# Optimization experiments

Measured on AMD Instinct MI355X. Metric: run time of the kernel, lower is better.

Reference implementation:

```python
import jax, jax.numpy as jnp
import numpy as np

# Model hyper-parameters (from CMRET __init__ defaults)
N_A, F, H, K, NK, L = 4096, 128, 4, 15, 50, 6
CUTOFF, TEMP, BOX, N_Z = 5.0, 2.0, 40.0, 100
DH = F // H  # per-head dim


def setup_inputs() -> dict:
    key = jax.random.key(0)
    ks = jax.random.split(key, 12)
    Z = jax.random.randint(ks[0], (1, N_A), 0, N_Z)
    R = jax.random.uniform(ks[1], (1, N_A, 3), dtype=jnp.float32) * BOX
    batch = jnp.ones((1, N_A, 1), jnp.float32)
    g = lambda k, shp, s: jax.random.normal(k, shp, jnp.float32) * s
    emb = g(ks[2], (N_Z, F), 1.0)
    Wq = g(ks[3], (L, F, F), F ** -0.5)
    Wk = g(ks[4], (L, F, F), F ** -0.5)
    Wv = g(ks[5], (L, F, 3 * F), F ** -0.5)
    We_k = g(ks[6], (L, NK, F), NK ** -0.5)
    be_k = jnp.zeros((L, F), jnp.float32)
    We_v = g(ks[7], (L, NK, 3 * F), NK ** -0.5)
    be_v = jnp.zeros((L, 3 * F), jnp.float32)
    ln_g = jnp.ones((F,), jnp.float32)
    ln_b = jnp.zeros((F,), jnp.float32)
    Wo1 = g(ks[8], (F, F), F ** -0.5)
    Wo2 = g(ks[9], (F, 1), F ** -0.5)
    return dict(Z=Z, R=R, batch=batch, emb=emb, Wq=Wq, Wk=Wk, Wv=Wv,
                We_k=We_k, be_k=be_k, We_v=We_v, be_v=be_v,
                ln_g=ln_g, ln_b=ln_b, Wo1=Wo1, Wo2=Wo2)


def reference(Z, R, batch, emb, Wq, Wk, Wv, We_k, be_k, We_v, be_v, ln_g, ln_b, Wo1, Wo2):
    n_a = Z.shape[1]
    r = R[0]                                  # (n_a, 3)
    b = batch[..., 0]                         # (1, n_a)
    bm = (b.T @ b) == 0                       # (n_a, n_a) cross-molecule mask
    # --- Distance: k-nearest-neighbour selection (gather-based) ---
    sq = jnp.sum(r * r, -1)
    d2 = sq[:, None] + sq[None, :] - 2.0 * (r @ r.T)
    d2 = jnp.where(bm | jnp.eye(n_a, dtype=bool), 1e9, jnp.maximum(d2, 0.0))
    _, idxs = jax.lax.top_k(-d2, K)           # (n_a, K) neighbour indices
    vec = r[idxs] - r[:, None, :]             # (n_a, K, 3)
    d = jnp.sqrt(jnp.sum(vec * vec, -1) + 1e-12)
    vec_norm = vec / d[..., None]
    # --- Gaussian RBF * cosine cutoff edge features ---
    mu = jnp.linspace(0.0, CUTOFF, NK, dtype=jnp.float32)
    delta = CUTOFF / NK
    cut = 0.5 * (jnp.cos(jnp.pi * d / CUTOFF) + 1.0) * (d <= CUTOFF)
    e = jnp.exp(-((d[..., None] - mu) ** 2) / (2.0 * delta * delta)) * cut[..., None]
    # --- embedding and channel init ---
    s = emb[Z[0]]                             # (n_a, F) scalar channel
    o = jnp.zeros_like(s)                     # residual accumulator
    v = jnp.zeros((n_a, 3, F), s.dtype)       # vector channel
    scale = jnp.asarray(1.0 / np.sqrt(DH * TEMP), jnp.float32)
    # --- attention interaction stack ---
    for l in range(L):
        q = (s @ Wq[l]).reshape(n_a, H, DH)
        kk = s @ Wk[l]
        val = s @ Wv[l]                       # (n_a, 3F)
        ek = jax.nn.silu(e @ We_k[l] + be_k[l])   # (n_a, K, F) edge key filter
        ev = jax.nn.silu(e @ We_v[l] + be_v[l])   # (n_a, K, 3F) edge value filter
        kh = (kk[idxs] * ek).reshape(n_a, K, H, DH)
        logits = jnp.einsum('nhd,nkhd->nkh', q, kh) * scale
        attn = jax.nn.softmax(logits, axis=1) * cut[..., None]
        wf = jnp.repeat(attn, DH, axis=-1)        # (n_a, K, F) per-channel weights
        m1, m2, m3 = jnp.split(val[idxs] * ev, 3, axis=-1)
        ds = jnp.sum(wf * m1, axis=1)             # scalar message (n_a, F)
        dv = jnp.sum((wf * m2)[:, :, None, :] * vec_norm[..., None]
                     + (wf * m3)[:, :, None, :] * v[idxs], axis=1)
        s = s + ds
        o = o + ds
        v = v + dv
    # --- final LayerNorm + readout ---
    mean = o.mean(-1, keepdims=True)
    var = o.var(-1, keepdims=True)
    o = (o - mean) / jnp.sqrt(var + 1e-5) * ln_g + ln_b
    h = jax.nn.silu(o @ Wo1) @ Wo2            # (n_a, 1) per-atom contribution
    return jnp.sum(h * batch[0], axis=0, keepdims=True)  # (1, 1) energy
```

## Files before the change

### kernel.cpp

```cpp
#include <hip/hip_runtime.h>
#include <math.h>

#define NATOMS  4096
#define FDIM    128
#define NHEAD   4
#define DHEAD   32
#define KNBR    15
#define NKER    50
#define NLAYER  6
#define QKVW    640
#define LISTCAP 768

typedef __attribute__((ext_vector_type(8))) short short8;
typedef __attribute__((ext_vector_type(4))) float f32x4;

__device__ __forceinline__ float silu_f(float x) { return x / (1.0f + __expf(-x)); }

__device__ __forceinline__ unsigned long long shfl_xor_u64(unsigned long long v, int m) {
    unsigned lo = (unsigned)v, hi = (unsigned)(v >> 32);
    lo = (unsigned)__shfl_xor((int)lo, m);
    hi = (unsigned)__shfl_xor((int)hi, m);
    return ((unsigned long long)hi << 32) | lo;
}
__device__ __forceinline__ unsigned long long min_u64(unsigned long long a, unsigned long long b) {
    return a < b ? a : b;
}
__device__ __forceinline__ int spread3(int v) {
    return (v & 1) | ((v & 2) << 2) | ((v & 4) << 4) | ((v & 8) << 6);
}

__global__ __launch_bounds__(1024) void morton_kernel(
    const float* __restrict__ R, const float* __restrict__ batch,
    int* __restrict__ perm, float* __restrict__ Rs,
    float* __restrict__ batch_s, int* __restrict__ cell_start)
{
    __shared__ int hist[4096];
    __shared__ int tscan[1024];
    const int t = threadIdx.x;
    int codes[4];
    float xs[4], ys[4], zs[4];
    #pragma unroll
    for (int u = 0; u < 4; ++u) hist[t*4 + u] = 0;
    __syncthreads();
    #pragma unroll
    for (int u = 0; u < 4; ++u) {
        int i = t + u*1024;
        float x = R[i*3+0], y = R[i*3+1], z = R[i*3+2];
        xs[u] = x; ys[u] = y; zs[u] = z;
        int cx = min(15, max(0, (int)(x * 0.4f)));
        int cy = min(15, max(0, (int)(y * 0.4f)));
        int cz = min(15, max(0, (int)(z * 0.4f)));
        int code = spread3(cx) | (spread3(cy) << 1) | (spread3(cz) << 2);
        codes[u] = code;
        atomicAdd(&hist[code], 1);
    }
    __syncthreads();
    int loc[4], s0 = 0;
    #pragma unroll
    for (int u = 0; u < 4; ++u) { loc[u] = hist[t*4 + u]; s0 += loc[u]; }
    tscan[t] = s0;
    __syncthreads();
    for (int off = 1; off < 1024; off <<= 1) {
        int v = tscan[t];
        int a = (t >= off) ? tscan[t - off] : 0;
        __syncthreads();
        tscan[t] = v + a;
        __syncthreads();
    }
    int run = tscan[t] - s0;
    #pragma unroll
    for (int u = 0; u < 4; ++u) {
        hist[t*4 + u] = run;
        cell_start[t*4 + u] = run;
        run += loc[u];
    }
    if (t == 0) cell_start[4096] = NATOMS;
    __syncthreads();
    #pragma unroll
    for (int u = 0; u < 4; ++u) {
        int i = t + u*1024;
        int r = atomicAdd(&hist[codes[u]], 1);
        perm[r] = i;
        Rs[r*3+0] = xs[u]; Rs[r*3+1] = ys[u]; Rs[r*3+2] = zs[u];
        batch_s[r] = batch[i];
    }
}

__global__ __launch_bounds__(64) void knn_kernel(
    const float* __restrict__ Rs, const float* __restrict__ batch_s,
    const int* __restrict__ cell_start,
    int* __restrict__ idxs, float* __restrict__ cutw,
    float* __restrict__ vecn, unsigned short* __restrict__ eA)
{
    __shared__ unsigned long long list[LISTCAP];
    __shared__ int   ridx[LISTCAP];
    __shared__ float e_lds[16][68];
    __shared__ float dist[KNBR];
    __shared__ float cutl[KNBR];
    __shared__ int   selr[KNBR];
    __shared__ int   cnt;
    const int r = blockIdx.x, t = threadIdx.x;
    if (t == 0) cnt = 0;
    for (int x = t; x < 16*68; x += 64) ((float*)e_lds)[x] = 0.0f;
    const float xi = Rs[r*3+0], yi = Rs[r*3+1], zi = Rs[r*3+2];
    const float bi = batch_s[r];
    const float sqi = xi*xi + yi*yi + zi*zi;
    const int cx = min(15, max(0, (int)(xi * 0.4f)));
    const int cy = min(15, max(0, (int)(yi * 0.4f)));
    const int cz = min(15, max(0, (int)(zi * 0.4f)));
    __syncthreads();

    for (int cid = t; cid < 343; cid += 64) {
        int nx = cx + (cid % 7) - 3;
        int ny = cy + ((cid / 7) % 7) - 3;
        int nz = cz + (cid / 49) - 3;
        if (nx < 0 || nx > 15 || ny < 0 || ny > 15 || nz < 0 || nz > 15) continue;
        int code = spread3(nx) | (spread3(ny) << 1) | (spread3(nz) << 2);
        int s0 = cell_start[code], s1 = cell_start[code + 1];
        for (int r2 = s0; r2 < s1; ++r2) {
            if (r2 == r) continue;
            float xj = Rs[r2*3+0], yj = Rs[r2*3+1], zj = Rs[r2*3+2];
            if (bi * batch_s[r2] == 0.0f) continue;
            float sqj = xj*xj + yj*yj + zj*zj;
            float d2 = sqi + sqj - 2.0f*(xi*xj + yi*yj + zi*zj);
            d2 = fmaxf(d2, 0.0f);
            int slot = atomicAdd(&cnt, 1);
            if (slot < LISTCAP) {
                list[slot] = ((unsigned long long)__float_as_uint(d2) << 32) | (unsigned)slot;
                ridx[slot] = r2;
            }
        }
    }
    __syncthreads();
    const int n = min(cnt, LISTCAP);

    unsigned long long cand = ~0ull;
    for (int idx = t; idx < n; idx += 64) cand = min_u64(cand, list[idx]);
    for (int k = 0; k < KNBR; ++k) {
        unsigned long long w = cand;
        #pragma unroll
        for (int off = 1; off < 64; off <<= 1)
            w = min_u64(w, shfl_xor_u64(w, off));
        int slot = (int)(unsigned)w;
        if (t == 0) selr[k] = ridx[slot];
        if ((slot & 63) == t) {
            list[slot] = ~0ull;
            cand = ~0ull;
            for (int idx = t; idx < n; idx += 64) cand = min_u64(cand, list[idx]);
        }
        __syncthreads();
    }

    if (t < KNBR) {
        int r2 = selr[t];
        idxs[r*KNBR + t] = r2;
        float vx = Rs[r2*3+0]-xi, vy = Rs[r2*3+1]-yi, vz = Rs[r2*3+2]-zi;
        float d = sqrtf(vx*vx + vy*vy + vz*vz + 1e-12f);
        float inv = 1.0f/d;
        vecn[(r*KNBR+t)*3+0] = vx*inv;
        vecn[(r*KNBR+t)*3+1] = vy*inv;
        vecn[(r*KNBR+t)*3+2] = vz*inv;
        const float PI = 3.14159265358979323846f;
        float cutv = (d <= 5.0f) ? 0.5f*(cosf(PI*d*0.2f) + 1.0f) : 0.0f;
        cutw[r*KNBR + t] = cutv;
        dist[t] = d; cutl[t] = cutv;
    }
    __syncthreads();

    for (int x = t; x < KNBR*NKER; x += 64) {
        int k = x / NKER, jj = x % NKER;
        float d = dist[k];
        float mu = 5.0f * (float)jj / 49.0f;
        float dd = d - mu;
        e_lds[k][jj] = __expf(-dd*dd*50.0f) * cutl[k];
    }
    __syncthreads();

    const int lx = t & 15, quad = t >> 4;
    #pragma unroll
    for (int grp = 0; grp < 4; ++grp) {
        const int ks = grp >> 1, part = grp & 1;
        short8 vv;
        #pragma unroll
        for (int j = 0; j < 8; ++j) {
            float v = e_lds[lx][ks*32 + quad*8 + j];
            unsigned b = __float_as_uint(v);
            if (part == 0) vv[j] = (short)(b >> 16);
            else {
                float rr = v - __uint_as_float(b & 0xFFFF0000u);
                vv[j] = (short)(__float_as_uint(rr) >> 16);
            }
        }
        *(short8*)(eA + (size_t)r*2048 + grp*512 + t*8) = vv;
    }
}

__global__ __launch_bounds__(256) void init_kernel(
    const int* __restrict__ Z, const float* __restrict__ emb,
    const int* __restrict__ perm,
    float* __restrict__ s, float* __restrict__ o, float* __restrict__ v0)
{
    int stride = gridDim.x * blockDim.x;
    for (int idx = blockIdx.x*blockDim.x + threadIdx.x; idx < NATOMS*3*FDIM; idx += stride) {
        v0[idx] = 0.0f;
        if (idx < NATOMS*FDIM) {
            int a = idx >> 7, c = idx & 127;
            s[idx] = emb[Z[perm[a]]*FDIM + c];
            o[idx] = 0.0f;
        }
    }
}

__global__ __launch_bounds__(64) void prep_kernel(
    const float* __restrict__ WeK, const float* __restrict__ WeV,
    const float* __restrict__ Wq, const float* __restrict__ Wk,
    const float* __restrict__ Wv,
    unsigned short* __restrict__ Wswz, unsigned short* __restrict__ Qswz)
{
    const int lane = threadIdx.x;
    if (blockIdx.x < NLAYER*32*2) {
        const int blk = blockIdx.x;
        const int ks = blk & 1;
        const int T  = (blk >> 1) & 31;
        const int l  = blk >> 6;
        const int quad = lane >> 4, x = lane & 15;
        unsigned short* dst = Wswz + (size_t)blk*1024 + lane*8;
        for (int j = 0; j < 8; ++j) {
            int k = ks*32 + quad*8 + j;
            float w = 0.0f;
            if (k < NKER)
                w = (T < 8) ? WeK[l*NKER*FDIM + k*FDIM + T*16 + x]
                            : WeV[(size_t)l*NKER*3*FDIM + k*3*FDIM + (T-8)*16 + x];
            unsigned b = __float_as_uint(w);
            dst[j] = (unsigned short)(b >> 16);
            float r = w - __uint_as_float(b & 0xFFFF0000u);
            dst[512 + j] = (unsigned short)(__float_as_uint(r) >> 16);
        }
    } else {
        const int blk = blockIdx.x - NLAYER*32*2;
        const int ks = blk & 3;
        const int ct = (blk >> 2) % 40;
        const int l  = blk / 160;
        const int quad = lane >> 4, lx = lane & 15;
        const int col = ct*16 + lx;
        unsigned short* dst = Qswz + (size_t)blk*1024 + lane*8;
        for (int j = 0; j < 8; ++j) {
            int k = ks*32 + quad*8 + j;
            float w;
            if (col < 128)      w = Wq[l*16384 + k*128 + col];
            else if (col < 256) w = Wk[l*16384 + k*128 + (col-128)];
            else                w = Wv[(size_t)l*49152 + k*384 + (col-256)];
            unsigned b = __float_as_uint(w);
            dst[j] = (unsigned short)(b >> 16);
            float r = w - __uint_as_float(b & 0xFFFF0000u);
            dst[512 + j] = (unsigned short)(__float_as_uint(r) >> 16);
        }
    }
}

__global__ __launch_bounds__(128) void proj_kernel(
    const float* __restrict__ S, const unsigned short* __restrict__ Qswz,
    float* __restrict__ QKV, int l)
{
    const int rt = blockIdx.x;
    const int t = threadIdx.x, wave = t >> 6, lane = t & 63;
    const int quad = lane >> 4, lx = lane & 15;
    const int cg = blockIdx.y*2 + wave;

    short8 ah[4], al[4];
    const float* srow = S + (size_t)(rt*16 + lx)*FDIM;
    #pragma unroll
    for (int ks = 0; ks < 4; ++ks) {
        float v[8];
        *(f32x4*)&v[0] = *(const f32x4*)(srow + ks*32 + quad*8);
        *(f32x4*)&v[4] = *(const f32x4*)(srow + ks*32 + quad*8 + 4);
        #pragma unroll
        for (int j = 0; j < 8; ++j) {
            unsigned b = __float_as_uint(v[j]);
            ah[ks][j] = (short)(b >> 16);
            float r = v[j] - __uint_as_float(b & 0xFFFF0000u);
            al[ks][j] = (short)(__float_as_uint(r) >> 16);
        }
    }
    for (int ci = 0; ci < 5; ++ci) {
        const int ct = cg*5 + ci;
        const unsigned short* wp = Qswz + (size_t)((l*40 + ct)*4)*1024 + lane*8;
        f32x4 acc = {0.0f, 0.0f, 0.0f, 0.0f};
        #pragma unroll
        for (int ks = 0; ks < 4; ++ks) {
            short8 bh = *(const short8*)(wp + ks*1024);
            short8 bl = *(const short8*)(wp + ks*1024 + 512);
            acc = __builtin_amdgcn_mfma_f32_16x16x32_bf16(ah[ks], bh, acc, 0, 0, 0);
            acc = __builtin_amdgcn_mfma_f32_16x16x32_bf16(ah[ks], bl, acc, 0, 0, 0);
            acc = __builtin_amdgcn_mfma_f32_16x16x32_bf16(al[ks], bh, acc, 0, 0, 0);
        }
        const int col = ct*16 + lx;
        #pragma unroll
        for (int r = 0; r < 4; ++r)
            QKV[(size_t)(rt*16 + quad*4 + r)*QKVW + col] = acc[r];
    }
}

__global__ __launch_bounds__(1024) void attn_kernel(
    const float* __restrict__ QKV, const int* __restrict__ idxs,
    const float* __restrict__ cutw, const float* __restrict__ vecn,
    const unsigned short* __restrict__ eA, const unsigned short* __restrict__ Wswz,
    const float* __restrict__ beK, const float* __restrict__ beV,
    float* __restrict__ s, float* __restrict__ o,
    const float* __restrict__ vin, float* __restrict__ vout, int l)
{
    __shared__ __align__(16) float fbuf[2][KNBR][513];
    __shared__ int   nidx[2][KNBR];
    __shared__ float cutv[2][KNBR];
    __shared__ float vnc[2][KNBR][3];
    __shared__ float attns[2][KNBR][NHEAD];

    const int t = threadIdx.x;
    const int half = t >> 9, tl = t & 511;
    const int i = blockIdx.x*2 + half;
    const int wave = tl >> 6, lane = t & 63;
    const int quad = lane >> 4, lx = lane & 15;

    if (tl < KNBR) {
        nidx[half][tl] = idxs[i*KNBR + tl];
        cutv[half][tl] = cutw[i*KNBR + tl];
        vnc[half][tl][0] = vecn[(i*KNBR+tl)*3+0];
        vnc[half][tl][1] = vecn[(i*KNBR+tl)*3+1];
        vnc[half][tl][2] = vecn[(i*KNBR+tl)*3+2];
    }
    const unsigned short* ea = eA + (size_t)i*2048 + lane*8;
    short8 eh[2], el[2];
    eh[0] = *(const short8*)(ea + 0*512);
    el[0] = *(const short8*)(ea + 1*512);
    eh[1] = *(const short8*)(ea + 2*512);
    el[1] = *(const short8*)(ea + 3*512);
    __syncthreads();

    #pragma unroll
    for (int tt = 0; tt < 4; ++tt) {
        const int T = wave*4 + tt;
        const int col = T*16 + lx;
        f32x4 acc = {0.0f, 0.0f, 0.0f, 0.0f};
        #pragma unroll
        for (int ks = 0; ks < 2; ++ks) {
            const unsigned short* wp = Wswz + ((size_t)((l*32+T)*2+ks))*1024 + lane*8;
            short8 bh = *(const short8*)wp;
            short8 bl = *(const short8*)(wp + 512);
            acc = __builtin_amdgcn_mfma_f32_16x16x32_bf16(eh[ks], bh, acc, 0, 0, 0);
            acc = __builtin_amdgcn_mfma_f32_16x16x32_bf16(eh[ks], bl, acc, 0, 0, 0);
            acc = __builtin_amdgcn_mfma_f32_16x16x32_bf16(el[ks], bh, acc, 0, 0, 0);
        }
        const float b = (col < FDIM) ? beK[l*FDIM + col]
                                     : beV[(size_t)l*3*FDIM + (col - FDIM)];
        const int goff = (col < FDIM) ? (FDIM + col) : (2*FDIM + (col - FDIM));
        #pragma unroll
        for (int r = 0; r < 4; ++r) {
            int k = quad*4 + r;
            if (k < KNBR) {
                float f = silu_f(acc[r] + b);
                float g = QKV[(size_t)nidx[half][k]*QKVW + goff];
                fbuf[half][k][col] = f * g;
            }
        }
    }
    __syncthreads();

    float pre[KNBR];
    if (tl < FDIM) {
        const int c = tl, h = c >> 5;
        const float q = QKV[(size_t)i*QKVW + c];
        float lg[KNBR];
        #pragma unroll
        for (int k = 0; k < KNBR; ++k) {
            float p = q * fbuf[half][k][c];
            p += __shfl_xor(p, 1);
            p += __shfl_xor(p, 2);
            p += __shfl_xor(p, 4);
            p += __shfl_xor(p, 8);
            p += __shfl_xor(p, 16);
            lg[k] = p * 0.125f;
        }
        float m = -1e30f;
        #pragma unroll
        for (int k = 0; k < KNBR; ++k) m = fmaxf(m, lg[k]);
        float ssum = 0.0f;
        #pragma unroll
        for (int k = 0; k < KNBR; ++k) { lg[k] = __expf(lg[k]-m); ssum += lg[k]; }
        float inv = 1.0f/ssum;
        if ((c & 31) == 0) {
            #pragma unroll
            for (int k = 0; k < KNBR; ++k) attns[half][k][h] = lg[k]*inv*cutv[half][k];
        }
    } else if (tl < 2*FDIM) {
        const int cc = tl - FDIM;
        #pragma unroll
        for (int k = 0; k < KNBR; ++k) pre[k] = fbuf[half][k][2*FDIM + cc];
    } else {
        const int cc = (tl < 3*FDIM) ? (tl - 2*FDIM) : (tl - 3*FDIM);
        #pragma unroll
        for (int k = 0; k < KNBR; ++k) pre[k] = fbuf[half][k][3*FDIM + cc];
    }
    __syncthreads();

    float d3[3] = {0.0f, 0.0f, 0.0f};
    if (tl < FDIM) {
        const int c = tl, h = c >> 5;
        float ds = 0.0f;
        #pragma unroll
        for (int k = 0; k < KNBR; ++k) ds += attns[half][k][h]*fbuf[half][k][FDIM + c];
        s[i*FDIM + c] += ds;
        o[i*FDIM + c] += ds;
    } else if (tl < 2*FDIM) {
        const int cc = tl - FDIM, h = cc >> 5;
        float d0 = 0.0f, d1 = 0.0f, d2 = 0.0f;
        #pragma unroll
        for (int k = 0; k < KNBR; ++k) {
            float w = attns[half][k][h]*pre[k];
            d0 += w*vnc[half][k][0]; d1 += w*vnc[half][k][1]; d2 += w*vnc[half][k][2];
        }
        fbuf[half][0][2*FDIM + cc] = d0;
        fbuf[half][1][2*FDIM + cc] = d1;
        fbuf[half][2][2*FDIM + cc] = d2;
    } else if (tl < 3*FDIM) {
        const int cc = tl - 2*FDIM, h = cc >> 5;
        #pragma unroll
        for (int k = 0; k < 8; ++k) {
            float w = attns[half][k][h]*pre[k];
            const float* vb = vin + (size_t)nidx[half][k]*3*FDIM + cc;
            d3[0] += w*vb[0*FDIM]; d3[1] += w*vb[1*FDIM]; d3[2] += w*vb[2*FDIM];
        }
    } else {
        const int cc = tl - 3*FDIM, h = cc >> 5;
        float e0 = 0.0f, e1 = 0.0f, e2 = 0.0f;
        #pragma unroll
        for (int k = 8; k < KNBR; ++k) {
            float w = attns[half][k][h]*pre[k];
            const float* vb = vin + (size_t)nidx[half][k]*3*FDIM + cc;
            e0 += w*vb[0*FDIM]; e1 += w*vb[1*FDIM]; e2 += w*vb[2*FDIM];
        }
        fbuf[half][3][2*FDIM + cc] = e0;
        fbuf[half][4][2*FDIM + cc] = e1;
        fbuf[half][5][2*FDIM + cc] = e2;
    }
    __syncthreads();

    if (tl >= 2*FDIM && tl < 3*FDIM) {
        const int cc = tl - 2*FDIM;
        #pragma unroll
        for (int x = 0; x < 3; ++x) {
            size_t off = (size_t)i*3*FDIM + x*FDIM + cc;
            vout[off] = vin[off] + fbuf[half][x][2*FDIM + cc]
                                 + fbuf[half][3+x][2*FDIM + cc] + d3[x];
        }
    }
}

__global__ __launch_bounds__(128) void final_kernel(
    const float* __restrict__ o, const float* __restrict__ lng, const float* __restrict__ lnb,
    const float* __restrict__ Wo1, const float* __restrict__ Wo2,
    const float* __restrict__ batch, const int* __restrict__ perm,
    float* __restrict__ hout)
{
    __shared__ float red[128];
    __shared__ float on[128];
    const int i = blockIdx.x, t = threadIdx.x;
    float x = o[i*FDIM + t];
    red[t] = x; __syncthreads();
    for (int off = 64; off > 0; off >>= 1) { if (t < off) red[t] += red[t+off]; __syncthreads(); }
    float mean = red[0] * (1.0f/128.0f);
    __syncthreads();
    float xm = x - mean;
    red[t] = xm*xm; __syncthreads();
    for (int off = 64; off > 0; off >>= 1) { if (t < off) red[t] += red[t+off]; __syncthreads(); }
    float var = red[0] * (1.0f/128.0f);
    __syncthreads();
    on[t] = xm * rsqrtf(var + 1e-5f) * lng[t] + lnb[t];
    __syncthreads();
    float acc = 0.0f;
    #pragma unroll 8
    for (int j = 0; j < 128; ++j) acc += on[j] * Wo1[j*128 + t];
    float h = silu_f(acc) * Wo2[t];
    red[t] = h; __syncthreads();
    for (int off = 64; off > 0; off >>= 1) { if (t < off) red[t] += red[t+off]; __syncthreads(); }
    if (t == 0) hout[i] = red[0] * batch[perm[i]];
}

__global__ __launch_bounds__(1024) void reduce_kernel(
    const float* __restrict__ hout, float* __restrict__ out)
{
    __shared__ float red[1024];
    const int t = threadIdx.x;
    float a = hout[t] + hout[t+1024] + hout[t+2048] + hout[t+3072];
    red[t] = a; __syncthreads();
    for (int off = 512; off > 0; off >>= 1) {
        if (t < off) red[t] += red[t+off];
        __syncthreads();
    }
    if (t == 0) out[0] = red[0];
}

extern "C" void kernel_launch(void* const* d_in, const int* in_sizes, int n_in,
                              void* d_out, int out_size, void* d_ws, size_t ws_size,
                              hipStream_t stream)
{
    const int*   Z     = (const int*)  d_in[0];
    const float* R     = (const float*)d_in[1];
    const float* batch = (const float*)d_in[2];
    const float* emb   = (const float*)d_in[3];
    const float* Wq    = (const float*)d_in[4];
    const float* Wk    = (const float*)d_in[5];
    const float* Wv    = (const float*)d_in[6];
    const float* WeK   = (const float*)d_in[7];
    const float* beK   = (const float*)d_in[8];
    const float* WeV   = (const float*)d_in[9];
    const float* beV   = (const float*)d_in[10];
    const float* lng   = (const float*)d_in[11];
    const float* lnb   = (const float*)d_in[12];
    const float* Wo1   = (const float*)d_in[13];
    const float* Wo2   = (const float*)d_in[14];
    float* out = (float*)d_out;

    float* fws = (float*)d_ws;
    float* s    = fws; fws += NATOMS*FDIM;
    float* o    = fws; fws += NATOMS*FDIM;
    float* v0   = fws; fws += NATOMS*3*FDIM;
    float* v1   = fws; fws += NATOMS*3*FDIM;
    float* qkv  = fws; fws += NATOMS*QKVW;
    float* cutw = fws; fws += NATOMS*KNBR;
    float* vecn = fws; fws += NATOMS*KNBR*3;
    float* hout = fws; fws += NATOMS;
    float* Rs   = fws; fws += NATOMS*3;
    float* bsrt = fws; fws += NATOMS;
    int*   idxs = (int*)fws; fws += NATOMS*KNBR;
    int*   perm = (int*)fws; fws += NATOMS;
    int*   cells= (int*)fws; fws += 4097;
    fws += 3;
    unsigned short* eA   = (unsigned short*)fws;
    fws += (NATOMS*2048) / 2;
    unsigned short* Wswz = (unsigned short*)fws;
    fws += (NLAYER*32*2*1024) / 2;
    unsigned short* Qswz = (unsigned short*)fws;

    morton_kernel<<<1, 1024, 0, stream>>>(R, batch, perm, Rs, bsrt, cells);
    prep_kernel<<<NLAYER*32*2 + NLAYER*40*4, 64, 0, stream>>>(WeK, WeV, Wq, Wk, Wv, Wswz, Qswz);
    knn_kernel<<<NATOMS, 64, 0, stream>>>(Rs, bsrt, cells, idxs, cutw, vecn, eA);
    init_kernel<<<1024, 256, 0, stream>>>(Z, emb, perm, s, o, v0);
    for (int l = 0; l < NLAYER; ++l) {
        proj_kernel<<<dim3(256, 4), 128, 0, stream>>>(s, Qswz, qkv, l);
        float* vin  = (l & 1) ? v1 : v0;
        float* vout = (l & 1) ? v0 : v1;
        attn_kernel<<<NATOMS/2, 1024, 0, stream>>>(qkv, idxs, cutw, vecn, eA, Wswz,
                                                   beK, beV, s, o, vin, vout, l);
    }
    final_kernel<<<NATOMS, 128, 0, stream>>>(o, lng, lnb, Wo1, Wo2, batch, perm, hout);
    reduce_kernel<<<1, 1024, 0, stream>>>(hout, out);
}
```

Baseline: 503.0 us.

## Use wave-level scans in morton/knn and re-split attention work per spatial component

The morton prefix scan now runs as a wave shuffle scan plus a 16-entry serial combine, replacing the 1024-wide LDS scan that needed many barriers. The knn candidate build becomes a two-pass count then wave prefix scan, so each thread writes to deterministic slots and the shared atomic counter goes away. The attention tail is reorganised so each group of 128 threads owns one vector component and does the full neighbour reduction itself, which removes the extra barrier and the LDS partial-sum exchange. It also pads fbuf to 516. The cost is that knn scans the cell lists twice, and the attention threads now load more per-neighbour data from registers and global memory.

Result: slower. 614.3 us (+22.1%).

```diff
diff --git a/kernel.cpp b/kernel.cpp
--- a/kernel.cpp
+++ b/kernel.cpp
@@ -10,6 +10,7 @@
 #define NLAYER  6
 #define QKVW    640
 #define LISTCAP 768
+#define FB      516
 
 typedef __attribute__((ext_vector_type(8))) short short8;
 typedef __attribute__((ext_vector_type(4))) float f32x4;
@@ -35,8 +36,9 @@
     float* __restrict__ batch_s, int* __restrict__ cell_start)
 {
     __shared__ int hist[4096];
-    __shared__ int tscan[1024];
+    __shared__ int wsum[16];
     const int t = threadIdx.x;
+    const int lane = t & 63, wave = t >> 6;
     int codes[4];
     float xs[4], ys[4], zs[4];
     #pragma unroll
@@ -58,16 +60,21 @@
     int loc[4], s0 = 0;
     #pragma unroll
     for (int u = 0; u < 4; ++u) { loc[u] = hist[t*4 + u]; s0 += loc[u]; }
-    tscan[t] = s0;
-    __syncthreads();
-    for (int off = 1; off < 1024; off <<= 1) {
-        int v = tscan[t];
-        int a = (t >= off) ? tscan[t - off] : 0;
-        __syncthreads();
-        tscan[t] = v + a;
-        __syncthreads();
-    }
-    int run = tscan[t] - s0;
+    int inc = s0;
+    #pragma unroll
+    for (int off = 1; off < 64; off <<= 1) {
+        int v = __shfl_up(inc, off);
+        if (lane >= off) inc += v;
+    }
+    if (lane == 63) wsum[wave] = inc;
+    __syncthreads();
+    if (t == 0) {
+        int running = 0;
+        #pragma unroll
+        for (int w = 0; w < 16; ++w) { int v = wsum[w]; wsum[w] = running; running += v; }
+    }
+    __syncthreads();
+    int run = wsum[wave] + inc - s0;
     #pragma unroll
     for (int u = 0; u < 4; ++u) {
         hist[t*4 + u] = run;
@@ -98,9 +105,7 @@
     __shared__ float dist[KNBR];
     __shared__ float cutl[KNBR];
     __shared__ int   selr[KNBR];
-    __shared__ int   cnt;
     const int r = blockIdx.x, t = threadIdx.x;
-    if (t == 0) cnt = 0;
     for (int x = t; x < 16*68; x += 64) ((float*)e_lds)[x] = 0.0f;
     const float xi = Rs[r*3+0], yi = Rs[r*3+1], zi = Rs[r*3+2];
     const float bi = batch_s[r];
@@ -108,8 +113,26 @@
     const int cx = min(15, max(0, (int)(xi * 0.4f)));
     const int cy = min(15, max(0, (int)(yi * 0.4f)));
     const int cz = min(15, max(0, (int)(zi * 0.4f)));
-    __syncthreads();
-
+
+    int nloc = 0;
+    for (int cid = t; cid < 343; cid += 64) {
+        int nx = cx + (cid % 7) - 3;
+        int ny = cy + ((cid / 7) % 7) - 3;
+        int nz = cz + (cid / 49) - 3;
+        if (nx < 0 || nx > 15 || ny < 0 || ny > 15 || nz < 0 || nz > 15) continue;
+        int code = spread3(nx) | (spread3(ny) << 1) | (spread3(nz) << 2);
+        int s0 = cell_start[code], s1 = cell_start[code + 1];
+        for (int r2 = s0; r2 < s1; ++r2)
+            if (r2 != r && bi * batch_s[r2] != 0.0f) nloc++;
+    }
+    int inc = nloc;
+    #pragma unroll
+    for (int off = 1; off < 64; off <<= 1) {
+        int v = __shfl_up(inc, off);
+        if (t >= off) inc += v;
+    }
+    const int total = __shfl(inc, 63);
+    int pos = inc - nloc;
     for (int cid = t; cid < 343; cid += 64) {
         int nx = cx + (cid % 7) - 3;
         int ny = cy + ((cid / 7) % 7) - 3;
@@ -118,21 +141,19 @@
         int code = spread3(nx) | (spread3(ny) << 1) | (spread3(nz) << 2);
         int s0 = cell_start[code], s1 = cell_start[code + 1];
         for (int r2 = s0; r2 < s1; ++r2) {
-            if (r2 == r) continue;
-            float xj = Rs[r2*3+0], yj = Rs[r2*3+1], zj = Rs[r2*3+2];
-            if (bi * batch_s[r2] == 0.0f) continue;
-            float sqj = xj*xj + yj*yj + zj*zj;
-            float d2 = sqi + sqj - 2.0f*(xi*xj + yi*yj + zi*zj);
-            d2 = fmaxf(d2, 0.0f);
-            int slot = atomicAdd(&cnt, 1);
-            if (slot < LISTCAP) {
-                list[slot] = ((unsigned long long)__float_as_uint(d2) << 32) | (unsigned)slot;
-                ridx[slot] = r2;
+            if (r2 == r || bi * batch_s[r2] == 0.0f) continue;
+            if (pos < LISTCAP) {
+                float xj = Rs[r2*3+0], yj = Rs[r2*3+1], zj = Rs[r2*3+2];
+                float sqj = xj*xj + yj*yj + zj*zj;
+                float d2 = fmaxf(sqi + sqj - 2.0f*(xi*xj + yi*yj + zi*zj), 0.0f);
+                list[pos] = ((unsigned long long)__float_as_uint(d2) << 32) | (unsigned)pos;
+                ridx[pos] = r2;
             }
-        }
-    }
-    __syncthreads();
-    const int n = min(cnt, LISTCAP);
+            pos++;
+        }
+    }
+    __syncthreads();
+    const int n = min(total, LISTCAP);
 
     unsigned long long cand = ~0ull;
     for (int idx = t; idx < n; idx += 64) cand = min_u64(cand, list[idx]);
@@ -309,7 +330,7 @@
     float* __restrict__ s, float* __restrict__ o,
     const float* __restrict__ vin, float* __restrict__ vout, int l)
 {
-    __shared__ __align__(16) float fbuf[2][KNBR][513];
+    __shared__ __align__(16) float fbuf[2][KNBR][FB];
     __shared__ int   nidx[2][KNBR];
     __shared__ float cutv[2][KNBR];
     __shared__ float vnc[2][KNBR][3];
@@ -365,14 +386,16 @@
     }
     __syncthreads();
 
-    float pre[KNBR];
-    if (tl < FDIM) {
-        const int c = tl, h = c >> 5;
-        const float q = QKV[(size_t)i*QKVW + c];
+    const int xg = tl >> 7;
+    const int cc = tl & 127;
+    const int h = cc >> 5;
+    float pre1[KNBR], pre2[KNBR], pre3[KNBR];
+    if (xg == 0) {
+        const float q = QKV[(size_t)i*QKVW + cc];
         float lg[KNBR];
         #pragma unroll
         for (int k = 0; k < KNBR; ++k) {
-            float p = q * fbuf[half][k][c];
+            float p = q * fbuf[half][k][cc];
             p += __shfl_xor(p, 1);
             p += __shfl_xor(p, 2);
             p += __shfl_xor(p, 4);
@@ -387,71 +410,37 @@
         #pragma unroll
         for (int k = 0; k < KNBR; ++k) { lg[k] = __expf(lg[k]-m); ssum += lg[k]; }
         float inv = 1.0f/ssum;
-        if ((c & 31) == 0) {
+        if ((cc & 31) == 0) {
             #pragma unroll
             for (int k = 0; k < KNBR; ++k) attns[half][k][h] = lg[k]*inv*cutv[half][k];
         }
-    } else if (tl < 2*FDIM) {
-        const int cc = tl - FDIM;
-        #pragma unroll
-        for (int k = 0; k < KNBR; ++k) pre[k] = fbuf[half][k][2*FDIM + cc];
+        #pragma unroll
+        for (int k = 0; k < KNBR; ++k) pre1[k] = fbuf[half][k][FDIM + cc];
     } else {
-        const int cc = (tl < 3*FDIM) ? (tl - 2*FDIM) : (tl - 3*FDIM);
-        #pragma unroll
-        for (int k = 0; k < KNBR; ++k) pre[k] = fbuf[half][k][3*FDIM + cc];
-    }
-    __syncthreads();
-
-    float d3[3] = {0.0f, 0.0f, 0.0f};
-    if (tl < FDIM) {
-        const int c = tl, h = c >> 5;
+        #pragma unroll
+        for (int k = 0; k < KNBR; ++k) pre2[k] = fbuf[half][k][2*FDIM + cc];
+        #pragma unroll
+        for (int k = 0; k < KNBR; ++k) pre3[k] = fbuf[half][k][3*FDIM + cc];
+    }
+    __syncthreads();
+
+    if (xg == 0) {
         float ds = 0.0f;
         #pragma unroll
-        for (int k = 0; k < KNBR; ++k) ds += attns[half][k][h]*fbuf[half][k][FDIM + c];
-        s[i*FDIM + c] += ds;
-        o[i*FDIM + c] += ds;
-    } else if (tl < 2*FDIM) {
-        const int cc = tl - FDIM, h = cc >> 5;
-        float d0 = 0.0f, d1 = 0.0f, d2 = 0.0f;
+        for (int k = 0; k < KNBR; ++k) ds += attns[half][k][h]*pre1[k];
+        s[i*FDIM + cc] += ds;
+        o[i*FDIM + cc] += ds;
+    } else {
+        const int x = xg - 1;
+        float dv = 0.0f;
         #pragma unroll
         for (int k = 0; k < KNBR; ++k) {
-            float w = attns[half][k][h]*pre[k];
-            d0 += w*vnc[half][k][0]; d1 += w*vnc[half][k][1]; d2 += w*vnc[half][k][2];
-        }
-        fbuf[half][0][2*FDIM + cc] = d0;
-        fbuf[half][1][2*FDIM + cc] = d1;
-        fbuf[half][2][2*FDIM + cc] = d2;
-    } else if (tl < 3*FDIM) {
-        const int cc = tl - 2*FDIM, h = cc >> 5;
-        #pragma unroll
-        for (int k = 0; k < 8; ++k) {
-            float w = attns[half][k][h]*pre[k];
-            const float* vb = vin + (size_t)nidx[half][k]*3*FDIM + cc;
-            d3[0] += w*vb[0*FDIM]; d3[1] += w*vb[1*FDIM]; d3[2] += w*vb[2*FDIM];
-        }
-    } else {
-        const int cc = tl - 3*FDIM, h = cc >> 5;
-        float e0 = 0.0f, e1 = 0.0f, e2 = 0.0f;
-        #pragma unroll
-        for (int k = 8; k < KNBR; ++k) {
-            float w = attns[half][k][h]*pre[k];
-            const float* vb = vin + (size_t)nidx[half][k]*3*FDIM + cc;
-            e0 += w*vb[0*FDIM]; e1 += w*vb[1*FDIM]; e2 += w*vb[2*FDIM];
-        }
-        fbuf[half][3][2*FDIM + cc] = e0;
-        fbuf[half][4][2*FDIM + cc] = e1;
-        fbuf[half][5][2*FDIM + cc] = e2;
-    }
-    __syncthreads();
-
-    if (tl >= 2*FDIM && tl < 3*FDIM) {
-        const int cc = tl - 2*FDIM;
-        #pragma unroll
-        for (int x = 0; x < 3; ++x) {
-            size_t off = (size_t)i*3*FDIM + x*FDIM + cc;
-            vout[off] = vin[off] + fbuf[half][x][2*FDIM + cc]
-                                 + fbuf[half][3+x][2*FDIM + cc] + d3[x];
-        }
+            float w = attns[half][k][h];
+            dv += w * (pre2[k]*vnc[half][k][x]
+                     + pre3[k]*vin[(size_t)nidx[half][k]*3*FDIM + x*FDIM + cc]);
+        }
+        size_t off = (size_t)i*3*FDIM + x*FDIM + cc;
+        vout[off] = vin[off] + dv;
     }
 }
 
```
